# Kernel optimization log

Measured on AMD Instinct MI355X. Metric: run time of the kernel, lower is better.

The kernel has to match this reference:

```python
import jax, jax.numpy as jnp
import numpy as np

EPS = 1e-6      # zero-token detection eps
LN_EPS = 1e-5   # torch LayerNorm default
H = 8           # num_heads


def setup_inputs() -> dict:
    key = jax.random.key(0)
    ks = jax.random.split(key, 6)
    B, T, D = 4, 2048, 512
    embs = jax.random.normal(ks[0], (B, T, D), jnp.float32)
    labels = jax.random.uniform(ks[1], (B, T), jnp.float32)
    s = 1.0 / np.sqrt(D)
    ln_g = jnp.ones((D,), jnp.float32)
    ln_b = jnp.zeros((D,), jnp.float32)
    in_proj_w = jax.random.uniform(ks[2], (3 * D, D), jnp.float32, -s, s)
    in_proj_b = jnp.zeros((3 * D,), jnp.float32)
    out_w = jax.random.uniform(ks[3], (D, D), jnp.float32, -s, s)
    out_b = jnp.zeros((D,), jnp.float32)
    alpha = jnp.float32(1.0)
    beta = jnp.float32(0.0)
    return {"embs": embs, "labels": labels, "ln_g": ln_g, "ln_b": ln_b,
            "in_proj_w": in_proj_w, "in_proj_b": in_proj_b,
            "out_w": out_w, "out_b": out_b, "alpha": alpha, "beta": beta}


def reference(embs, labels, ln_g, ln_b, in_proj_w, in_proj_b, out_w, out_b, alpha, beta):
    B, T, D = embs.shape
    h, dh = H, D // H
    # pre-LayerNorm
    mu = embs.mean(-1, keepdims=True)
    var = ((embs - mu) ** 2).mean(-1, keepdims=True)
    x = (embs - mu) / jnp.sqrt(var + LN_EPS) * ln_g + ln_b
    # key padding mask from all-zero tokens (computed on normalized x, as in source)
    kpm = jnp.abs(x).sum(-1) <= EPS                      # [B,T] bool
    w = jnp.where(kpm, jnp.float32(0.0), labels)         # zero labels on masked tokens
    # fused qkv projection (nn.MultiheadAttention in_proj)
    qkv = x @ in_proj_w.T + in_proj_b                    # [B,T,3D]
    q, k, v = jnp.split(qkv, 3, axis=-1)
    def sp(a):
        return a.reshape(B, T, h, dh).transpose(0, 2, 1, 3)  # [B,h,T,dh]
    q, k, v = sp(q), sp(k), sp(v)
    scores = jnp.einsum('bhqd,bhkd->bhqk', q, k) / np.sqrt(dh)
    # additive label bias: alpha * labels (broadcast over heads & queries) + beta
    scores = scores + (alpha * w[:, None, None, :] + beta)
    # key padding mask -> -inf (use large negative for stability)
    scores = jnp.where(kpm[:, None, None, :], jnp.float32(-1e30), scores)
    a = jax.nn.softmax(scores, axis=-1)
    o = jnp.einsum('bhqk,bhkd->bhqd', a, v).transpose(0, 2, 1, 3).reshape(B, T, D)
    o = o @ out_w.T + out_b
    o = jnp.nan_to_num(o, nan=0.0, posinf=0.0, neginf=0.0)
    # masked mean pool over T
    m = (~kpm)[..., None].astype(o.dtype)                # [B,T,1]
    pooled = (o * m).sum(1) / jnp.maximum(m.sum(1), 1.0)  # [B,D]
    return pooled
```

## Files before the change

### kernel.cpp

```cpp
#include <hip/hip_runtime.h>
#include <math.h>

#define T 2048
#define D 512
#define NH 8
#define DH 64
#define NB 4
#define NTOK (NB * T)
#define LOG2E 1.44269504f
#define QSCALE (0.125f * LOG2E)

using bf16x8 = __attribute__((ext_vector_type(8))) short;
using f32x4  = __attribute__((ext_vector_type(4))) float;

static __device__ __forceinline__ unsigned short f2bf(float f) {
    union { float f; unsigned u; } v; v.f = f;
    unsigned r = v.u + 0x7fffu + ((v.u >> 16) & 1u);
    return (unsigned short)(r >> 16);
}
#if __has_builtin(__builtin_amdgcn_cvt_pk_bf16_f32)
static __device__ __forceinline__ unsigned pack_bf16_pair(float a, float b) {
    auto r = __builtin_amdgcn_cvt_pk_bf16_f32(a, b);
    union { decltype(r) v; unsigned u; } c; c.v = r;
    return c.u;
}
#else
static __device__ __forceinline__ unsigned pack_bf16_pair(float a, float b) {
    union { float f; unsigned u; } ua, ub; ua.f = a; ub.f = b;
    unsigned ra = ua.u + 0x7fffu + ((ua.u >> 16) & 1u);
    unsigned rb = ub.u + 0x7fffu + ((ub.u >> 16) & 1u);
    return __builtin_amdgcn_perm(rb, ra, 0x07060302);
}
#endif


__global__ __launch_bounds__(256) void prep_kernel(
    const float* __restrict__ embs, const float* __restrict__ labels,
    const float* __restrict__ g, const float* __restrict__ bb,
    const float* __restrict__ alpha_p, const float* __restrict__ beta_p,
    const float* __restrict__ ipw,
    unsigned short* __restrict__ xfrag, float* __restrict__ wexp,
    float* __restrict__ kpmf, unsigned short* __restrict__ wbfrag,
    float* __restrict__ S)
{
    __shared__ __align__(16) unsigned short Sh[16][520];
    int blk = blockIdx.x;
    int tid = threadIdx.x, wave = tid >> 6, lane = tid & 63;
    int quad = lane >> 4, lm = lane & 15;

    if (blk >= 608) {
        float4 z = {0.f, 0.f, 0.f, 0.f};
        ((float4*)S)[tid] = z;
        ((float4*)S)[tid + 256] = z;
        return;
    }

    if (blk < 512) {
        int t16 = blk;
        float4 g0 = *(const float4*)(g + lane * 8), g1 = *(const float4*)(g + lane * 8 + 4);
        float4 c0 = *(const float4*)(bb + lane * 8), c1 = *(const float4*)(bb + lane * 8 + 4);
        float gv[8] = {g0.x, g0.y, g0.z, g0.w, g1.x, g1.y, g1.z, g1.w};
        float cv[8] = {c0.x, c0.y, c0.z, c0.w, c1.x, c1.y, c1.z, c1.w};

        for (int tt = 0; tt < 4; ++tt) {
            int n = t16 * 16 + wave * 4 + tt;
            const float* e = embs + (size_t)n * D + lane * 8;
            float4 a4 = *(const float4*)e, b4 = *(const float4*)(e + 4);
            float v[8] = {a4.x, a4.y, a4.z, a4.w, b4.x, b4.y, b4.z, b4.w};

            float s = 0.f, ss = 0.f;
            #pragma unroll
            for (int j = 0; j < 8; ++j) { s += v[j]; ss += v[j] * v[j]; }
            #pragma unroll
            for (int o = 1; o <= 32; o <<= 1) {
                s += __shfl_xor(s, o, 64);
                ss += __shfl_xor(ss, o, 64);
            }
            float mu = s * (1.0f / D);
            float var = ss * (1.0f / D) - mu * mu;
            float rstd = rsqrtf(var + 1e-5f);

            float x[8], as = 0.f;
            #pragma unroll
            for (int j = 0; j < 8; ++j) {
                x[j] = (v[j] - mu) * rstd * gv[j] + cv[j];
                as += fabsf(x[j]);
            }
            uint4 pk;
            pk.x = pack_bf16_pair(x[0], x[1]);
            pk.y = pack_bf16_pair(x[2], x[3]);
            pk.z = pack_bf16_pair(x[4], x[5]);
            pk.w = pack_bf16_pair(x[6], x[7]);
            *(uint4*)&Sh[wave * 4 + tt][lane * 8] = pk;

            #pragma unroll
            for (int o = 1; o <= 32; o <<= 1) as += __shfl_xor(as, o, 64);
            if (lane == 0) {
                int kpm = (as <= 1e-6f);
                kpmf[n] = kpm ? 1.0f : 0.0f;
                wexp[n] = kpm ? 0.0f : __expf(alpha_p[0] * labels[n] + beta_p[0]);
            }
        }
        __syncthreads();
        #pragma unroll
        for (int i = 0; i < 4; ++i) {
            int kc = wave * 4 + i;
            bf16x8 fr = *(const bf16x8*)&Sh[lm][kc * 32 + quad * 8];
            *(bf16x8*)(xfrag + ((size_t)(t16 * 16 + kc) * 64 + lane) * 8) = fr;
        }
    } else {
        int j16 = blk - 512;
        for (int tt = 0; tt < 4; ++tt) {
            int j = j16 * 16 + wave * 4 + tt;
            const float* wp = ipw + (size_t)j * D + lane * 8;
            float4 a4 = *(const float4*)wp, b4 = *(const float4*)(wp + 4);
            uint4 pk;
            pk.x = pack_bf16_pair(a4.x, a4.y);
            pk.y = pack_bf16_pair(a4.z, a4.w);
            pk.z = pack_bf16_pair(b4.x, b4.y);
            pk.w = pack_bf16_pair(b4.z, b4.w);
            *(uint4*)&Sh[wave * 4 + tt][lane * 8] = pk;
        }
        __syncthreads();
        #pragma unroll
        for (int i = 0; i < 4; ++i) {
            int kc = wave * 4 + i;
            bf16x8 fr = *(const bf16x8*)&Sh[lm][kc * 32 + quad * 8];
            *(bf16x8*)(wbfrag + ((size_t)(j16 * 16 + kc) * 64 + lane) * 8) = fr;
        }
    }
}

__global__ __launch_bounds__(256) void qkv_mfma(
    const unsigned short* __restrict__ xfrag, const unsigned short* __restrict__ wbfrag,
    const float* __restrict__ bias, const float* __restrict__ wexp,
    unsigned short* __restrict__ qfrag, unsigned short* __restrict__ kfrag,
    unsigned short* __restrict__ vfrag)
{
    __shared__ __align__(16) unsigned short Ls[4][64][72];
    int tid = threadIdx.x;
    int wave = tid >> 6, lane = tid & 63, quad = lane >> 4, lm = lane & 15;
    int wr = wave >> 1, wc = wave & 1;
    int bid = blockIdx.x;
    int xcd = bid & 7, i = bid >> 3;
    int mblk = xcd * 8 + (i & 7);
    int jblk = i >> 3;
    int m0 = mblk * 128 + wr * 64;
    int j0 = jblk * 128 + wc * 64;
    int mt16 = m0 >> 4, jt16 = j0 >> 4;

    f32x4 acc[4][4];
    #pragma unroll
    for (int a = 0; a < 4; ++a)
        #pragma unroll
        for (int b = 0; b < 4; ++b) acc[a][b] = (f32x4){0.f,0.f,0.f,0.f};

    bf16x8 af0[4], bf0[4], af1[4], bf1[4];
    auto load_ab = [&](int kc, bf16x8 (&af)[4], bf16x8 (&bf)[4]) {
        #pragma unroll
        for (int mf = 0; mf < 4; ++mf)
            af[mf] = *(const bf16x8*)(xfrag + ((size_t)((mt16 + mf) * 16 + kc) * 64 + lane) * 8);
        #pragma unroll
        for (int nt = 0; nt < 4; ++nt)
            bf[nt] = *(const bf16x8*)(wbfrag + ((size_t)((jt16 + nt) * 16 + kc) * 64 + lane) * 8);
    };
    auto do_mfma = [&](bf16x8 (&af)[4], bf16x8 (&bf)[4]) {
        #pragma unroll
        for (int mf = 0; mf < 4; ++mf)
            #pragma unroll
            for (int nt = 0; nt < 4; ++nt)
                acc[mf][nt] = __builtin_amdgcn_mfma_f32_16x16x32_bf16(af[mf], bf[nt], acc[mf][nt], 0, 0, 0);
    };

    load_ab(0, af0, bf0);
    for (int kc = 0; kc < 16; kc += 2) {
        load_ab(kc + 1, af1, bf1);
        do_mfma(af0, bf0);
        load_ab((kc + 2) & 15, af0, bf0);
        do_mfma(af1, bf1);
    }

    int part = j0 >> 9;
    int h = (j0 & 511) >> 6;
    int b_ = m0 >> 11, tloc = m0 & (T - 1);
    int bh = b_ * NH + h;
    float bcol[4];
    #pragma unroll
    for (int nt = 0; nt < 4; ++nt) bcol[nt] = bias[j0 + nt * 16 + lm];

    if (part == 2) {
        float wv[4][4];
        #pragma unroll
        for (int mf = 0; mf < 4; ++mf)
            #pragma unroll
            for (int r = 0; r < 4; ++r)
                wv[mf][r] = wexp[b_ * T + tloc + mf * 16 + quad * 4 + r];
        #pragma unroll
        for (int mf = 0; mf < 4; ++mf)
            #pragma unroll
            for (int nt = 0; nt < 4; ++nt) {
                uint2 pw;
                pw.x = pack_bf16_pair((acc[mf][nt][0] + bcol[nt]) * wv[mf][0],
                                      (acc[mf][nt][1] + bcol[nt]) * wv[mf][1]);
                pw.y = pack_bf16_pair((acc[mf][nt][2] + bcol[nt]) * wv[mf][2],
                                      (acc[mf][nt][3] + bcol[nt]) * wv[mf][3]);
                *(uint2*)&Ls[wave][nt * 16 + lm][mf * 16 + quad * 4] = pw;
            }
        #pragma unroll
        for (int nt = 0; nt < 4; ++nt)
            #pragma unroll
            for (int kk = 0; kk < 2; ++kk) {
                bf16x8 fr = *(const bf16x8*)&Ls[wave][nt * 16 + lm][kk * 32 + quad * 8];
                size_t chunk = ((((size_t)bh * 32 + (tloc >> 6)) * 2 + kk) * 5) + nt;
                *(bf16x8*)(vfrag + chunk * 512 + lane * 8) = fr;
            }
        #pragma unroll
        for (int kk = 0; kk < 2; ++kk) {
            size_t chunk = ((((size_t)bh * 32 + (tloc >> 6)) * 2 + kk) * 5) + 4;
            uint4 pk = {0u, 0u, 0u, 0u};
            if (lm == 0) {
                const float* wp = wexp + b_ * T + tloc + kk * 32 + quad * 8;
                unsigned short vv[8];
                #pragma unroll
                for (int e = 0; e < 8; ++e) vv[e] = f2bf(wp[e]);
                pk = *(uint4*)vv;
            }
            *(uint4*)(vfrag + chunk * 512 + (size_t)lane * 8) = pk;
        }
    } else {
        float scale = (part == 0) ? QSCALE : 1.0f;
        #pragma unroll
        for (int mf = 0; mf < 4; ++mf)
            #pragma unroll
            for (int nt = 0; nt < 4; ++nt)
                #pragma unroll
                for (int r = 0; r < 4; ++r)
                    Ls[wave][mf * 16 + quad * 4 + r][nt * 16 + lm] =
                        f2bf((acc[mf][nt][r] + bcol[nt]) * scale);
        if (part == 0) {
            #pragma unroll
            for (int mf = 0; mf < 4; ++mf)
                #pragma unroll
                for (int kk = 0; kk < 2; ++kk) {
                    bf16x8 fr = *(const bf16x8*)&Ls[wave][mf * 16 + lm][kk * 32 + quad * 8];
                    size_t chunk = ((size_t)bh * 128 + (tloc >> 4) + mf) * 2 + kk;
                    *(bf16x8*)(qfrag + chunk * 512 + lane * 8) = fr;
                }
        } else {
            #pragma unroll
            for (int nta = 0; nta < 4; ++nta)
                #pragma unroll
                for (int kk = 0; kk < 2; ++kk) {
                    bf16x8 fr = *(const bf16x8*)&Ls[wave][lm * 4 + nta][kk * 32 + quad * 8];
                    size_t chunk = ((((size_t)bh * 32 + (tloc >> 6)) * 2 + kk) * 4) + nta;
                    *(bf16x8*)(kfrag + chunk * 512 + lane * 8) = fr;
                }
        }
    }
}

__global__ __launch_bounds__(256, 2) void attn_mfma(
    const unsigned short* __restrict__ qfrag, const unsigned short* __restrict__ kfrag,
    const unsigned short* __restrict__ vfrag, const float* __restrict__ kpmf,
    float* __restrict__ S)
{
    __shared__ __align__(16) unsigned short Ps[4][2][64][72];
    __shared__ float Lx[2][2][64];
    int g = blockIdx.x;
    int bh = g & 31, q0 = (g >> 5) * 128;
    int tid = threadIdx.x, wave = tid >> 6, lane = tid & 63;
    int quad = lane >> 4, lm = lane & 15;
    int qh = wave >> 1, ks = wave & 1;
    int qbase = q0 + qh * 64;
    int b_ = bh >> 3, h = bh & 7;

    bf16x8 qf[4][2];
    int t16b = (qbase >> 4);
    #pragma unroll
    for (int mf = 0; mf < 4; ++mf)
        #pragma unroll
        for (int kk = 0; kk < 2; ++kk)
            qf[mf][kk] = *(const bf16x8*)(qfrag +
                (((size_t)(bh * 128 + t16b + mf) * 2 + kk) * 64 + lane) * 8);

    f32x4 accO[4][4], accL[4];
    #pragma unroll
    for (int mf = 0; mf < 4; ++mf) {
        #pragma unroll
        for (int nt = 0; nt < 4; ++nt) accO[mf][nt] = (f32x4){0.f,0.f,0.f,0.f};
        accL[mf] = (f32x4){0.f,0.f,0.f,0.f};
    }

    const unsigned short* kb = kfrag + (size_t)bh * 32 * 8 * 512 + (size_t)lane * 8;
    const unsigned short* vb = vfrag + (size_t)bh * 32 * 10 * 512 + (size_t)lane * 8;
    int t0k = ks * 16;

    bf16x8 kf[4][2];
    auto load_k = [&](int t64) {
        const unsigned short* p = kb + (size_t)t64 * 8 * 512;
        #pragma unroll
        for (int kk = 0; kk < 2; ++kk)
            #pragma unroll
            for (int nt = 0; nt < 4; ++nt)
                kf[nt][kk] = *(const bf16x8*)(p + ((size_t)kk * 4 + nt) * 512);
    };
    auto load_v = [&](int t64, bf16x8 (&vf)[5][2]) {
        const unsigned short* p = vb + (size_t)t64 * 10 * 512;
        #pragma unroll
        for (int kk = 0; kk < 2; ++kk)
            #pragma unroll
            for (int nt = 0; nt < 5; ++nt)
                vf[nt][kk] = *(const bf16x8*)(p + ((size_t)kk * 5 + nt) * 512);
    };
    auto load_p = [&](int buf, bf16x8 (&pf)[4][2]) {
        #pragma unroll
        for (int mf = 0; mf < 4; ++mf)
            #pragma unroll
            for (int kk = 0; kk < 2; ++kk)
                pf[mf][kk] = *(const bf16x8*)&Ps[wave][buf][mf * 16 + lm][kk * 32 + quad * 8];
    };
    auto qk_exp = [&](int buf) {
        #pragma unroll
        for (int mf = 0; mf < 4; ++mf) {
            f32x4 s[4];
            __builtin_amdgcn_s_setprio(1);
            #pragma unroll
            for (int nt = 0; nt < 4; ++nt) {
                f32x4 t0 = (f32x4){0.f,0.f,0.f,0.f};
                t0 = __builtin_amdgcn_mfma_f32_16x16x32_bf16(qf[mf][0], kf[nt][0], t0, 0, 0, 0);
                t0 = __builtin_amdgcn_mfma_f32_16x16x32_bf16(qf[mf][1], kf[nt][1], t0, 0, 0, 0);
                s[nt] = t0;
            }
            __builtin_amdgcn_s_setprio(0);
            int rowb = mf * 16 + quad * 4;
            #pragma unroll
            for (int r = 0; r < 4; ++r) {
                float p0 = __builtin_amdgcn_exp2f(s[0][r]);
                float p1 = __builtin_amdgcn_exp2f(s[1][r]);
                float p2 = __builtin_amdgcn_exp2f(s[2][r]);
                float p3 = __builtin_amdgcn_exp2f(s[3][r]);
                uint2 pw;
                pw.x = pack_bf16_pair(p0, p1);
                pw.y = pack_bf16_pair(p2, p3);
                *(uint2*)&Ps[wave][buf][rowb + r][lm * 4] = pw;
            }
        }
    };
    auto pv = [&](bf16x8 (&pf)[4][2], bf16x8 (&vf)[5][2]) {
        __builtin_amdgcn_s_setprio(1);
        #pragma unroll
        for (int mf = 0; mf < 4; ++mf) {
            #pragma unroll
            for (int nt = 0; nt < 4; ++nt) {
                accO[mf][nt] = __builtin_amdgcn_mfma_f32_16x16x32_bf16(pf[mf][0], vf[nt][0], accO[mf][nt], 0, 0, 0);
                accO[mf][nt] = __builtin_amdgcn_mfma_f32_16x16x32_bf16(pf[mf][1], vf[nt][1], accO[mf][nt], 0, 0, 0);
            }
            accL[mf] = __builtin_amdgcn_mfma_f32_16x16x32_bf16(pf[mf][0], vf[4][0], accL[mf], 0, 0, 0);
            accL[mf] = __builtin_amdgcn_mfma_f32_16x16x32_bf16(pf[mf][1], vf[4][1], accL[mf], 0, 0, 0);
        }
        __builtin_amdgcn_s_setprio(0);
    };

    load_k(t0k);
    qk_exp(0);
    load_k(t0k + 1);
    for (int t = 1; t < 16; ++t) {
        bf16x8 pf[4][2], vf[5][2];
        load_p((t - 1) & 1, pf);
        load_v(t0k + t - 1, vf);
        qk_exp(t & 1);
        load_k(t0k + ((t + 1) & 15));
        pv(pf, vf);
    }
    {
        bf16x8 pf[4][2], vf[5][2];
        load_p(1, pf);
        load_v(t0k + 15, vf);
        pv(pf, vf);
    }

    if (lm == 0) {
        #pragma unroll
        for (int mf = 0; mf < 4; ++mf)
            #pragma unroll
            for (int r = 0; r < 4; ++r)
                Lx[qh][ks][mf * 16 + quad * 4 + r] = accL[mf][r];
    }
    __syncthreads();

    float pooled[4] = {0.f, 0.f, 0.f, 0.f};
    #pragma unroll
    for (int mf = 0; mf < 4; ++mf)
        #pragma unroll
        for (int r = 0; r < 4; ++r) {
            int rloc = mf * 16 + quad * 4 + r;
            float l = Lx[qh][0][rloc] + Lx[qh][1][rloc];
            float w = (1.0f - kpmf[b_ * T + qbase + rloc]) / l;
            #pragma unroll
            for (int nt = 0; nt < 4; ++nt) pooled[nt] += accO[mf][nt][r] * w;
        }
    #pragma unroll
    for (int nt = 0; nt < 4; ++nt) {
        pooled[nt] += __shfl_xor(pooled[nt], 16, 64);
        pooled[nt] += __shfl_xor(pooled[nt], 32, 64);
    }
    if (quad == 0) {
        #pragma unroll
        for (int nt = 0; nt < 4; ++nt)
            atomicAdd(&S[b_ * D + h * DH + nt * 16 + lm], pooled[nt]);
    }
}

__global__ __launch_bounds__(256) void out_kernel(
    const float* __restrict__ S, const float* __restrict__ kpmf,
    const float* __restrict__ Wo, const float* __restrict__ bo,
    float* __restrict__ out)
{
    __shared__ float Sl[512];
    __shared__ float cs[4];
    __shared__ float pr[4][64];
    int b_ = blockIdx.x >> 3;
    int cg = blockIdx.x & 7;
    int tid = threadIdx.x;
    int col = tid & 63, kq = tid >> 6;
    Sl[tid] = S[b_ * D + tid];
    Sl[tid + 256] = S[b_ * D + tid + 256];
    const float* kp = kpmf + b_ * T;
    float c = 0.f;
    for (int t = tid; t < T; t += 256) c += kp[t];
    #pragma unroll
    for (int o = 32; o; o >>= 1) c += __shfl_xor(c, o, 64);
    if ((tid & 63) == 0) cs[tid >> 6] = c;
    __syncthreads();
    float masked = cs[0] + cs[1] + cs[2] + cs[3];
    float cnt = (float)T - masked;
    float inv = 1.0f / fmaxf(cnt, 1.0f);

    int d = cg * 64 + col;
    const float4* wr4 = (const float4*)(Wo + (size_t)d * D + kq * 128);
    float dot = 0.f;
    #pragma unroll 8
    for (int i = 0; i < 32; ++i) {
        float4 w4 = wr4[i];
        int kbase = kq * 128 + i * 4;
        dot += Sl[kbase + 0] * w4.x + Sl[kbase + 1] * w4.y +
               Sl[kbase + 2] * w4.z + Sl[kbase + 3] * w4.w;
    }
    pr[kq][col] = dot;
    __syncthreads();
    if (kq == 0) {
        float tot = pr[0][col] + pr[1][col] + pr[2][col] + pr[3][col];
        out[b_ * D + d] = (tot + bo[d] * cnt) * inv;
    }
}

extern "C" void kernel_launch(void* const* d_in, const int* in_sizes, int n_in,
                              void* d_out, int out_size, void* d_ws, size_t ws_size,
                              hipStream_t stream) {
    const float* embs   = (const float*)d_in[0];
    const float* labels = (const float*)d_in[1];
    const float* ln_g   = (const float*)d_in[2];
    const float* ln_b   = (const float*)d_in[3];
    const float* ipw    = (const float*)d_in[4];
    const float* ipb    = (const float*)d_in[5];
    const float* ow     = (const float*)d_in[6];
    const float* obb    = (const float*)d_in[7];
    const float* alpha  = (const float*)d_in[8];
    const float* beta   = (const float*)d_in[9];
    float* out = (float*)d_out;

    unsigned short* xfrag  = (unsigned short*)d_ws;
    unsigned short* wbfrag = xfrag + (size_t)NTOK * D;
    unsigned short* qfrag  = wbfrag + (size_t)3 * D * D;
    unsigned short* kfrag  = qfrag + (size_t)NTOK * D;
    unsigned short* vfrag  = kfrag + (size_t)NTOK * D;
    float* wexp = (float*)(vfrag + (size_t)32 * 32 * 2 * 5 * 512);
    float* kpmf = wexp + NTOK;
    float* S    = kpmf + NTOK;

    prep_kernel<<<609, 256, 0, stream>>>(embs, labels, ln_g, ln_b, alpha, beta,
                                         ipw, xfrag, wexp, kpmf, wbfrag, S);
    qkv_mfma<<<768, 256, 0, stream>>>(xfrag, wbfrag, ipb, wexp, qfrag, kfrag, vfrag);
    attn_mfma<<<32 * (T / 128), 256, 0, stream>>>(qfrag, kfrag, vfrag, kpmf, S);
    out_kernel<<<NB * 8, 256, 0, stream>>>(S, kpmf, ow, obb, out);
}
```

Baseline: 153.2 us.

## Fuse four kernels into one persistent mega-kernel with global barriers

Merges the prep, QKV GEMM, attention and output-projection kernels into a single 512-block launch. Stages are separated by atomic-counter grid barriers, and one LDS union is shared across the stages. The QKV stage assigns 1.5 tiles per block, so blocks below 256 do a second unit. The aim is to remove kernel launch gaps and inter-kernel drain/fill. The risks are deadlock if not all 512 blocks are co-resident, imbalance in the QKV stage, and barrier spin overhead; it also adds a memset.

```diff
diff --git a/kernel.cpp b/kernel.cpp
--- a/kernel.cpp
+++ b/kernel.cpp
@@ -34,28 +34,47 @@
 #endif
 
 
-__global__ __launch_bounds__(256) void prep_kernel(
+struct AttnLds { unsigned short Ps[4][2][64][72]; float Lx[2][2][64]; };
+struct OutLds  { float Sl[512]; float cs[4]; float pr[4][64]; };
+union MegaLds {
+    unsigned short Sh[16][520];
+    unsigned short Ls[4][64][72];
+    AttnLds at;
+    OutLds  op;
+};
+
+__global__ __launch_bounds__(256, 2) void mega_kernel(
     const float* __restrict__ embs, const float* __restrict__ labels,
     const float* __restrict__ g, const float* __restrict__ bb,
     const float* __restrict__ alpha_p, const float* __restrict__ beta_p,
-    const float* __restrict__ ipw,
-    unsigned short* __restrict__ xfrag, float* __restrict__ wexp,
-    float* __restrict__ kpmf, unsigned short* __restrict__ wbfrag,
-    float* __restrict__ S)
+    const float* __restrict__ ipw, const float* __restrict__ ipb,
+    const float* __restrict__ ow, const float* __restrict__ obb,
+    unsigned short* __restrict__ xfrag, unsigned short* __restrict__ wbfrag,
+    unsigned short* __restrict__ qfrag, unsigned short* __restrict__ kfrag,
+    unsigned short* __restrict__ vfrag,
+    float* __restrict__ wexp, float* __restrict__ kpmf,
+    float* S, int* cnt, float* __restrict__ out)
 {
-    __shared__ __align__(16) unsigned short Sh[16][520];
+    __shared__ __align__(16) MegaLds u;
     int blk = blockIdx.x;
     int tid = threadIdx.x, wave = tid >> 6, lane = tid & 63;
     int quad = lane >> 4, lm = lane & 15;
 
-    if (blk >= 608) {
-        float4 z = {0.f, 0.f, 0.f, 0.f};
-        ((float4*)S)[tid] = z;
-        ((float4*)S)[tid + 256] = z;
-        return;
-    }
-
-    if (blk < 512) {
+    auto gsync = [&](int idx, bool wait) {
+        __syncthreads();
+        __threadfence();
+        if (tid == 0) {
+            __hip_atomic_fetch_add(&cnt[idx], 1, __ATOMIC_ACQ_REL, __HIP_MEMORY_SCOPE_AGENT);
+            if (wait) {
+                while (__hip_atomic_load(&cnt[idx], __ATOMIC_ACQUIRE, __HIP_MEMORY_SCOPE_AGENT) < 512)
+                    __builtin_amdgcn_s_sleep(8);
+            }
+        }
+        __syncthreads();
+        __threadfence();
+    };
+
+    {
         int t16 = blk;
         float4 g0 = *(const float4*)(g + lane * 8), g1 = *(const float4*)(g + lane * 8 + 4);
         float4 c0 = *(const float4*)(bb + lane * 8), c1 = *(const float4*)(bb + lane * 8 + 4);
@@ -91,7 +110,7 @@
             pk.y = pack_bf16_pair(x[2], x[3]);
             pk.z = pack_bf16_pair(x[4], x[5]);
             pk.w = pack_bf16_pair(x[6], x[7]);
-            *(uint4*)&Sh[wave * 4 + tt][lane * 8] = pk;
+            *(uint4*)&u.Sh[wave * 4 + tt][lane * 8] = pk;
 
             #pragma unroll
             for (int o = 1; o <= 32; o <<= 1) as += __shfl_xor(as, o, 64);
@@ -105,352 +124,337 @@
         #pragma unroll
         for (int i = 0; i < 4; ++i) {
             int kc = wave * 4 + i;
-            bf16x8 fr = *(const bf16x8*)&Sh[lm][kc * 32 + quad * 8];
+            bf16x8 fr = *(const bf16x8*)&u.Sh[lm][kc * 32 + quad * 8];
             *(bf16x8*)(xfrag + ((size_t)(t16 * 16 + kc) * 64 + lane) * 8) = fr;
         }
-    } else {
-        int j16 = blk - 512;
-        for (int tt = 0; tt < 4; ++tt) {
-            int j = j16 * 16 + wave * 4 + tt;
-            const float* wp = ipw + (size_t)j * D + lane * 8;
-            float4 a4 = *(const float4*)wp, b4 = *(const float4*)(wp + 4);
-            uint4 pk;
-            pk.x = pack_bf16_pair(a4.x, a4.y);
-            pk.y = pack_bf16_pair(a4.z, a4.w);
-            pk.z = pack_bf16_pair(b4.x, b4.y);
-            pk.w = pack_bf16_pair(b4.z, b4.w);
-            *(uint4*)&Sh[wave * 4 + tt][lane * 8] = pk;
-        }
-        __syncthreads();
-        #pragma unroll
-        for (int i = 0; i < 4; ++i) {
-            int kc = wave * 4 + i;
-            bf16x8 fr = *(const bf16x8*)&Sh[lm][kc * 32 + quad * 8];
-            *(bf16x8*)(wbfrag + ((size_t)(j16 * 16 + kc) * 64 + lane) * 8) = fr;
+
+        if (blk < 96) {
+            __syncthreads();
+            int j16 = blk;
+            for (int tt = 0; tt < 4; ++tt) {
+                int j = j16 * 16 + wave * 4 + tt;
+                const float* wp = ipw + (size_t)j * D + lane * 8;
+                float4 a4 = *(const float4*)wp, b4 = *(const float4*)(wp + 4);
+                uint4 pk;
+                pk.x = pack_bf16_pair(a4.x, a4.y);
+                pk.y = pack_bf16_pair(a4.z, a4.w);
+                pk.z = pack_bf16_pair(b4.x, b4.y);
+                pk.w = pack_bf16_pair(b4.z, b4.w);
+                *(uint4*)&u.Sh[wave * 4 + tt][lane * 8] = pk;
+            }
+            __syncthreads();
+            #pragma unroll
+            for (int i = 0; i < 4; ++i) {
+                int kc = wave * 4 + i;
+                bf16x8 fr = *(const bf16x8*)&u.Sh[lm][kc * 32 + quad * 8];
+                *(bf16x8*)(wbfrag + ((size_t)(j16 * 16 + kc) * 64 + lane) * 8) = fr;
+            }
         }
     }
-}
-
-__global__ __launch_bounds__(256) void qkv_mfma(
-    const unsigned short* __restrict__ xfrag, const unsigned short* __restrict__ wbfrag,
-    const float* __restrict__ bias, const float* __restrict__ wexp,
-    unsigned short* __restrict__ qfrag, unsigned short* __restrict__ kfrag,
-    unsigned short* __restrict__ vfrag)
-{
-    __shared__ __align__(16) unsigned short Ls[4][64][72];
-    int tid = threadIdx.x;
-    int wave = tid >> 6, lane = tid & 63, quad = lane >> 4, lm = lane & 15;
-    int wr = wave >> 1, wc = wave & 1;
-    int bid = blockIdx.x;
-    int xcd = bid & 7, i = bid >> 3;
-    int mblk = xcd * 8 + (i & 7);
-    int jblk = i >> 3;
-    int m0 = mblk * 128 + wr * 64;
-    int j0 = jblk * 128 + wc * 64;
-    int mt16 = m0 >> 4, jt16 = j0 >> 4;
-
-    f32x4 acc[4][4];
-    #pragma unroll
-    for (int a = 0; a < 4; ++a)
-        #pragma unroll
-        for (int b = 0; b < 4; ++b) acc[a][b] = (f32x4){0.f,0.f,0.f,0.f};
-
-    bf16x8 af0[4], bf0[4], af1[4], bf1[4];
-    auto load_ab = [&](int kc, bf16x8 (&af)[4], bf16x8 (&bf)[4]) {
+    gsync(0, true);
+
+    {
+        int wr = wave >> 1, wc = wave & 1;
+        auto qkv_unit = [&](int unit) {
+            int xcd = unit & 7, i = unit >> 3;
+            int mblk = xcd * 8 + (i & 7);
+            int jblk = i >> 3;
+            int m0 = mblk * 128 + wr * 64;
+            int j0 = jblk * 128 + wc * 64;
+            int mt16 = m0 >> 4, jt16 = j0 >> 4;
+
+            f32x4 acc[4][4];
+            #pragma unroll
+            for (int a = 0; a < 4; ++a)
+                #pragma unroll
+                for (int b = 0; b < 4; ++b) acc[a][b] = (f32x4){0.f,0.f,0.f,0.f};
+
+            bf16x8 af0[4], bf0[4], af1[4], bf1[4];
+            auto load_ab = [&](int kc, bf16x8 (&af)[4], bf16x8 (&bf)[4]) {
+                #pragma unroll
+                for (int mf = 0; mf < 4; ++mf)
+                    af[mf] = *(const bf16x8*)(xfrag + ((size_t)((mt16 + mf) * 16 + kc) * 64 + lane) * 8);
+                #pragma unroll
+                for (int nt = 0; nt < 4; ++nt)
+                    bf[nt] = *(const bf16x8*)(wbfrag + ((size_t)((jt16 + nt) * 16 + kc) * 64 + lane) * 8);
+            };
+            auto do_mfma = [&](bf16x8 (&af)[4], bf16x8 (&bf)[4]) {
+                #pragma unroll
+                for (int mf = 0; mf < 4; ++mf)
+                    #pragma unroll
+                    for (int nt = 0; nt < 4; ++nt)
+                        acc[mf][nt] = __builtin_amdgcn_mfma_f32_16x16x32_bf16(af[mf], bf[nt], acc[mf][nt], 0, 0, 0);
+            };
+
+            load_ab(0, af0, bf0);
+            for (int kc = 0; kc < 16; kc += 2) {
+                load_ab(kc + 1, af1, bf1);
+                do_mfma(af0, bf0);
+                load_ab((kc + 2) & 15, af0, bf0);
+                do_mfma(af1, bf1);
+            }
+
+            int part = j0 >> 9;
+            int h = (j0 & 511) >> 6;
+            int b_ = m0 >> 11, tloc = m0 & (T - 1);
+            int bh = b_ * NH + h;
+            float bcol[4];
+            #pragma unroll
+            for (int nt = 0; nt < 4; ++nt) bcol[nt] = ipb[j0 + nt * 16 + lm];
+
+            if (part == 2) {
+                float wv[4][4];
+                #pragma unroll
+                for (int mf = 0; mf < 4; ++mf)
+                    #pragma unroll
+                    for (int r = 0; r < 4; ++r)
+                        wv[mf][r] = wexp[b_ * T + tloc + mf * 16 + quad * 4 + r];
+                #pragma unroll
+                for (int mf = 0; mf < 4; ++mf)
+                    #pragma unroll
+                    for (int nt = 0; nt < 4; ++nt) {
+                        uint2 pw;
+                        pw.x = pack_bf16_pair((acc[mf][nt][0] + bcol[nt]) * wv[mf][0],
+                                              (acc[mf][nt][1] + bcol[nt]) * wv[mf][1]);
+                        pw.y = pack_bf16_pair((acc[mf][nt][2] + bcol[nt]) * wv[mf][2],
+                                              (acc[mf][nt][3] + bcol[nt]) * wv[mf][3]);
+                        *(uint2*)&u.Ls[wave][nt * 16 + lm][mf * 16 + quad * 4] = pw;
+                    }
+                #pragma unroll
+                for (int nt = 0; nt < 4; ++nt)
+                    #pragma unroll
+                    for (int kk = 0; kk < 2; ++kk) {
+                        bf16x8 fr = *(const bf16x8*)&u.Ls[wave][nt * 16 + lm][kk * 32 + quad * 8];
+                        size_t chunk = ((((size_t)bh * 32 + (tloc >> 6)) * 2 + kk) * 5) + nt;
+                        *(bf16x8*)(vfrag + chunk * 512 + lane * 8) = fr;
+                    }
+                #pragma unroll
+                for (int kk = 0; kk < 2; ++kk) {
+                    size_t chunk = ((((size_t)bh * 32 + (tloc >> 6)) * 2 + kk) * 5) + 4;
+                    uint4 pk = {0u, 0u, 0u, 0u};
+                    if (lm == 0) {
+                        const float* wp = wexp + b_ * T + tloc + kk * 32 + quad * 8;
+                        unsigned short vv[8];
+                        #pragma unroll
+                        for (int e = 0; e < 8; ++e) vv[e] = f2bf(wp[e]);
+                        pk = *(uint4*)vv;
+                    }
+                    *(uint4*)(vfrag + chunk * 512 + (size_t)lane * 8) = pk;
+                }
+            } else {
+                float scale = (part == 0) ? QSCALE : 1.0f;
+                #pragma unroll
+                for (int mf = 0; mf < 4; ++mf)
+                    #pragma unroll
+                    for (int nt = 0; nt < 4; ++nt)
+                        #pragma unroll
+                        for (int r = 0; r < 4; ++r)
+                            u.Ls[wave][mf * 16 + quad * 4 + r][nt * 16 + lm] =
+                                f2bf((acc[mf][nt][r] + bcol[nt]) * scale);
+                if (part == 0) {
+                    #pragma unroll
+                    for (int mf = 0; mf < 4; ++mf)
+                        #pragma unroll
+                        for (int kk = 0; kk < 2; ++kk) {
+                            bf16x8 fr = *(const bf16x8*)&u.Ls[wave][mf * 16 + lm][kk * 32 + quad * 8];
+                            size_t chunk = ((size_t)bh * 128 + (tloc >> 4) + mf) * 2 + kk;
+                            *(bf16x8*)(qfrag + chunk * 512 + lane * 8) = fr;
+                        }
+                } else {
+                    #pragma unroll
+                    for (int nta = 0; nta < 4; ++nta)
+                        #pragma unroll
+                        for (int kk = 0; kk < 2; ++kk) {
+                            bf16x8 fr = *(const bf16x8*)&u.Ls[wave][lm * 4 + nta][kk * 32 + quad * 8];
+                            size_t chunk = ((((size_t)bh * 32 + (tloc >> 6)) * 2 + kk) * 4) + nta;
+                            *(bf16x8*)(kfrag + chunk * 512 + lane * 8) = fr;
+                        }
+                }
+            }
+        };
+        qkv_unit(blk);
+        if (blk < 256) { __syncthreads(); qkv_unit(blk + 512); }
+    }
+    gsync(1, true);
+
+    {
+        int bh = blk & 31, q0 = (blk >> 5) * 128;
+        int qh = wave >> 1, ks = wave & 1;
+        int qbase = q0 + qh * 64;
+        int b_ = bh >> 3, h = bh & 7;
+
+        bf16x8 qf[4][2];
+        int t16b = (qbase >> 4);
         #pragma unroll
         for (int mf = 0; mf < 4; ++mf)
-            af[mf] = *(const bf16x8*)(xfrag + ((size_t)((mt16 + mf) * 16 + kc) * 64 + lane) * 8);
-        #pragma unroll
-        for (int nt = 0; nt < 4; ++nt)
-            bf[nt] = *(const bf16x8*)(wbfrag + ((size_t)((jt16 + nt) * 16 + kc) * 64 + lane) * 8);
-    };
-    auto do_mfma = [&](bf16x8 (&af)[4], bf16x8 (&bf)[4]) {
+            #pragma unroll
+            for (int kk = 0; kk < 2; ++kk)
+                qf[mf][kk] = *(const bf16x8*)(qfrag +
+                    (((size_t)(bh * 128 + t16b + mf) * 2 + kk) * 64 + lane) * 8);
+
+        f32x4 accO[4][4], accL[4];
+        #pragma unroll
+        for (int mf = 0; mf < 4; ++mf) {
+            #pragma unroll
+            for (int nt = 0; nt < 4; ++nt) accO[mf][nt] = (f32x4){0.f,0.f,0.f,0.f};
+            accL[mf] = (f32x4){0.f,0.f,0.f,0.f};
+        }
+
+        const unsigned short* kb = kfrag + (size_t)bh * 32 * 8 * 512 + (size_t)lane * 8;
+        const unsigned short* vb = vfrag + (size_t)bh * 32 * 10 * 512 + (size_t)lane * 8;
+        int t0k = ks * 16;
+
+        bf16x8 kf[4][2];
+        auto load_k = [&](int t64) {
+            const unsigned short* p = kb + (size_t)t64 * 8 * 512;
+            #pragma unroll
+            for (int kk = 0; kk < 2; ++kk)
+                #pragma unroll
+                for (int nt = 0; nt < 4; ++nt)
+                    kf[nt][kk] = *(const bf16x8*)(p + ((size_t)kk * 4 + nt) * 512);
+        };
+        auto load_v = [&](int t64, bf16x8 (&vf)[5][2]) {
+            const unsigned short* p = vb + (size_t)t64 * 10 * 512;
+            #pragma unroll
+            for (int kk = 0; kk < 2; ++kk)
+                #pragma unroll
+                for (int nt = 0; nt < 5; ++nt)
+                    vf[nt][kk] = *(const bf16x8*)(p + ((size_t)kk * 5 + nt) * 512);
+        };
+        auto load_p = [&](int buf, bf16x8 (&pf)[4][2]) {
+            #pragma unroll
+            for (int mf = 0; mf < 4; ++mf)
+                #pragma unroll
+                for (int kk = 0; kk < 2; ++kk)
+                    pf[mf][kk] = *(const bf16x8*)&u.at.Ps[wave][buf][mf * 16 + lm][kk * 32 + quad * 8];
+        };
+        auto qk_exp = [&](int buf) {
+            #pragma unroll
+            for (int mf = 0; mf < 4; ++mf) {
+                f32x4 s[4];
+                __builtin_amdgcn_s_setprio(1);
+                #pragma unroll
+                for (int nt = 0; nt < 4; ++nt) {
+                    f32x4 t0 = (f32x4){0.f,0.f,0.f,0.f};
+                    t0 = __builtin_amdgcn_mfma_f32_16x16x32_bf16(qf[mf][0], kf[nt][0], t0, 0, 0, 0);
+                    t0 = __builtin_amdgcn_mfma_f32_16x16x32_bf16(qf[mf][1], kf[nt][1], t0, 0, 0, 0);
+                    s[nt] = t0;
+                }
+                __builtin_amdgcn_s_setprio(0);
+                int rowb = mf * 16 + quad * 4;
+                #pragma unroll
+                for (int r = 0; r < 4; ++r) {
+                    float p0 = __builtin_amdgcn_exp2f(s[0][r]);
+                    float p1 = __builtin_amdgcn_exp2f(s[1][r]);
+                    float p2 = __builtin_amdgcn_exp2f(s[2][r]);
+                    float p3 = __builtin_amdgcn_exp2f(s[3][r]);
+                    uint2 pw;
+                    pw.x = pack_bf16_pair(p0, p1);
+                    pw.y = pack_bf16_pair(p2, p3);
+                    *(uint2*)&u.at.Ps[wave][buf][rowb + r][lm * 4] = pw;
+                }
+            }
+        };
+        auto pv = [&](bf16x8 (&pf)[4][2], bf16x8 (&vf)[5][2]) {
+            __builtin_amdgcn_s_setprio(1);
+            #pragma unroll
+            for (int mf = 0; mf < 4; ++mf) {
+                #pragma unroll
+                for (int nt = 0; nt < 4; ++nt) {
+                    accO[mf][nt] = __builtin_amdgcn_mfma_f32_16x16x32_bf16(pf[mf][0], vf[nt][0], accO[mf][nt], 0, 0, 0);
+                    accO[mf][nt] = __builtin_amdgcn_mfma_f32_16x16x32_bf16(pf[mf][1], vf[nt][1], accO[mf][nt], 0, 0, 0);
+                }
+                accL[mf] = __builtin_amdgcn_mfma_f32_16x16x32_bf16(pf[mf][0], vf[4][0], accL[mf], 0, 0, 0);
+                accL[mf] = __builtin_amdgcn_mfma_f32_16x16x32_bf16(pf[mf][1], vf[4][1], accL[mf], 0, 0, 0);
+            }
+            __builtin_amdgcn_s_setprio(0);
+        };
+
+        load_k(t0k);
+        qk_exp(0);
+        load_k(t0k + 1);
+        for (int t = 1; t < 16; ++t) {
+            bf16x8 pf[4][2], vf[5][2];
+            load_p((t - 1) & 1, pf);
+            load_v(t0k + t - 1, vf);
+            qk_exp(t & 1);
+            load_k(t0k + ((t + 1) & 15));
+            pv(pf, vf);
+        }
+        {
+            bf16x8 pf[4][2], vf[5][2];
+            load_p(1, pf);
+            load_v(t0k + 15, vf);
+            pv(pf, vf);
+        }
+
+        if (lm == 0) {
+            #pragma unroll
+            for (int mf = 0; mf < 4; ++mf)
+                #pragma unroll
+                for (int r = 0; r < 4; ++r)
+                    u.at.Lx[qh][ks][mf * 16 + quad * 4 + r] = accL[mf][r];
+        }
+        __syncthreads();
+
+        float pooled[4] = {0.f, 0.f, 0.f, 0.f};
         #pragma unroll
         for (int mf = 0; mf < 4; ++mf)
             #pragma unroll
+            for (int r = 0; r < 4; ++r) {
+                int rloc = mf * 16 + quad * 4 + r;
+                float l = u.at.Lx[qh][0][rloc] + u.at.Lx[qh][1][rloc];
+                float w = (1.0f - kpmf[b_ * T + qbase + rloc]) / l;
+                #pragma unroll
+                for (int nt = 0; nt < 4; ++nt) pooled[nt] += accO[mf][nt][r] * w;
+            }
+        #pragma unroll
+        for (int nt = 0; nt < 4; ++nt) {
+            pooled[nt] += __shfl_xor(pooled[nt], 16, 64);
+            pooled[nt] += __shfl_xor(pooled[nt], 32, 64);
+        }
+        if (quad == 0) {
+            #pragma unroll
             for (int nt = 0; nt < 4; ++nt)
-                acc[mf][nt] = __builtin_amdgcn_mfma_f32_16x16x32_bf16(af[mf], bf[nt], acc[mf][nt], 0, 0, 0);
-    };
-
-    load_ab(0, af0, bf0);
-    for (int kc = 0; kc < 16; kc += 2) {
-        load_ab(kc + 1, af1, bf1);
-        do_mfma(af0, bf0);
-        load_ab((kc + 2) & 15, af0, bf0);
-        do_mfma(af1, bf1);
+                atomicAdd(&S[b_ * D + h * DH + nt * 16 + lm], pooled[nt]);
+        }
     }
 
-    int part = j0 >> 9;
-    int h = (j0 & 511) >> 6;
-    int b_ = m0 >> 11, tloc = m0 & (T - 1);
-    int bh = b_ * NH + h;
-    float bcol[4];
-    #pragma unroll
-    for (int nt = 0; nt < 4; ++nt) bcol[nt] = bias[j0 + nt * 16 + lm];
-
-    if (part == 2) {
-        float wv[4][4];
-        #pragma unroll
-        for (int mf = 0; mf < 4; ++mf)
-            #pragma unroll
-            for (int r = 0; r < 4; ++r)
-                wv[mf][r] = wexp[b_ * T + tloc + mf * 16 + quad * 4 + r];
-        #pragma unroll
-        for (int mf = 0; mf < 4; ++mf)
-            #pragma unroll
-            for (int nt = 0; nt < 4; ++nt) {
-                uint2 pw;
-                pw.x = pack_bf16_pair((acc[mf][nt][0] + bcol[nt]) * wv[mf][0],
-                                      (acc[mf][nt][1] + bcol[nt]) * wv[mf][1]);
-                pw.y = pack_bf16_pair((acc[mf][nt][2] + bcol[nt]) * wv[mf][2],
-                                      (acc[mf][nt][3] + bcol[nt]) * wv[mf][3]);
-                *(uint2*)&Ls[wave][nt * 16 + lm][mf * 16 + quad * 4] = pw;
-            }
-        #pragma unroll
-        for (int nt = 0; nt < 4; ++nt)
-            #pragma unroll
-            for (int kk = 0; kk < 2; ++kk) {
-                bf16x8 fr = *(const bf16x8*)&Ls[wave][nt * 16 + lm][kk * 32 + quad * 8];
-                size_t chunk = ((((size_t)bh * 32 + (tloc >> 6)) * 2 + kk) * 5) + nt;
-                *(bf16x8*)(vfrag + chunk * 512 + lane * 8) = fr;
-            }
-        #pragma unroll
-        for (int kk = 0; kk < 2; ++kk) {
-            size_t chunk = ((((size_t)bh * 32 + (tloc >> 6)) * 2 + kk) * 5) + 4;
-            uint4 pk = {0u, 0u, 0u, 0u};
-            if (lm == 0) {
-                const float* wp = wexp + b_ * T + tloc + kk * 32 + quad * 8;
-                unsigned short vv[8];
-                #pragma unroll
-                for (int e = 0; e < 8; ++e) vv[e] = f2bf(wp[e]);
-                pk = *(uint4*)vv;
-            }
-            *(uint4*)(vfrag + chunk * 512 + (size_t)lane * 8) = pk;
-        }
-    } else {
-        float scale = (part == 0) ? QSCALE : 1.0f;
-        #pragma unroll
-        for (int mf = 0; mf < 4; ++mf)
-            #pragma unroll
-            for (int nt = 0; nt < 4; ++nt)
-                #pragma unroll
-                for (int r = 0; r < 4; ++r)
-                    Ls[wave][mf * 16 + quad * 4 + r][nt * 16 + lm] =
-                        f2bf((acc[mf][nt][r] + bcol[nt]) * scale);
-        if (part == 0) {
-            #pragma unroll
-            for (int mf = 0; mf < 4; ++mf)
-                #pragma unroll
-                for (int kk = 0; kk < 2; ++kk) {
-                    bf16x8 fr = *(const bf16x8*)&Ls[wave][mf * 16 + lm][kk * 32 + quad * 8];
-                    size_t chunk = ((size_t)bh * 128 + (tloc >> 4) + mf) * 2 + kk;
-                    *(bf16x8*)(qfrag + chunk * 512 + lane * 8) = fr;
-                }
-        } else {
-            #pragma unroll
-            for (int nta = 0; nta < 4; ++nta)
-                #pragma unroll
-                for (int kk = 0; kk < 2; ++kk) {
-                    bf16x8 fr = *(const bf16x8*)&Ls[wave][lm * 4 + nta][kk * 32 + quad * 8];
-                    size_t chunk = ((((size_t)bh * 32 + (tloc >> 6)) * 2 + kk) * 4) + nta;
-                    *(bf16x8*)(kfrag + chunk * 512 + lane * 8) = fr;
-                }
-        }
-    }
-}
-
-__global__ __launch_bounds__(256, 2) void attn_mfma(
-    const unsigned short* __restrict__ qfrag, const unsigned short* __restrict__ kfrag,
-    const unsigned short* __restrict__ vfrag, const float* __restrict__ kpmf,
-    float* __restrict__ S)
-{
-    __shared__ __align__(16) unsigned short Ps[4][2][64][72];
-    __shared__ float Lx[2][2][64];
-    int g = blockIdx.x;
-    int bh = g & 31, q0 = (g >> 5) * 128;
-    int tid = threadIdx.x, wave = tid >> 6, lane = tid & 63;
-    int quad = lane >> 4, lm = lane & 15;
-    int qh = wave >> 1, ks = wave & 1;
-    int qbase = q0 + qh * 64;
-    int b_ = bh >> 3, h = bh & 7;
-
-    bf16x8 qf[4][2];
-    int t16b = (qbase >> 4);
-    #pragma unroll
-    for (int mf = 0; mf < 4; ++mf)
-        #pragma unroll
-        for (int kk = 0; kk < 2; ++kk)
-            qf[mf][kk] = *(const bf16x8*)(qfrag +
-                (((size_t)(bh * 128 + t16b + mf) * 2 + kk) * 64 + lane) * 8);
-
-    f32x4 accO[4][4], accL[4];
-    #pragma unroll
-    for (int mf = 0; mf < 4; ++mf) {
-        #pragma unroll
-        for (int nt = 0; nt < 4; ++nt) accO[mf][nt] = (f32x4){0.f,0.f,0.f,0.f};
-        accL[mf] = (f32x4){0.f,0.f,0.f,0.f};
-    }
-
-    const unsigned short* kb = kfrag + (size_t)bh * 32 * 8 * 512 + (size_t)lane * 8;
-    const unsigned short* vb = vfrag + (size_t)bh * 32 * 10 * 512 + (size_t)lane * 8;
-    int t0k = ks * 16;
-
-    bf16x8 kf[4][2];
-    auto load_k = [&](int t64) {
-        const unsigned short* p = kb + (size_t)t64 * 8 * 512;
-        #pragma unroll
-        for (int kk = 0; kk < 2; ++kk)
-            #pragma unroll
-            for (int nt = 0; nt < 4; ++nt)
-                kf[nt][kk] = *(const bf16x8*)(p + ((size_t)kk * 4 + nt) * 512);
-    };
-    auto load_v = [&](int t64, bf16x8 (&vf)[5][2]) {
-        const unsigned short* p = vb + (size_t)t64 * 10 * 512;
-        #pragma unroll
-        for (int kk = 0; kk < 2; ++kk)
-            #pragma unroll
-            for (int nt = 0; nt < 5; ++nt)
-                vf[nt][kk] = *(const bf16x8*)(p + ((size_t)kk * 5 + nt) * 512);
-    };
-    auto load_p = [&](int buf, bf16x8 (&pf)[4][2]) {
-        #pragma unroll
-        for (int mf = 0; mf < 4; ++mf)
-            #pragma unroll
-            for (int kk = 0; kk < 2; ++kk)
-                pf[mf][kk] = *(const bf16x8*)&Ps[wave][buf][mf * 16 + lm][kk * 32 + quad * 8];
-    };
-    auto qk_exp = [&](int buf) {
-        #pragma unroll
-        for (int mf = 0; mf < 4; ++mf) {
-            f32x4 s[4];
-            __builtin_amdgcn_s_setprio(1);
-            #pragma unroll
-            for (int nt = 0; nt < 4; ++nt) {
-                f32x4 t0 = (f32x4){0.f,0.f,0.f,0.f};
-                t0 = __builtin_amdgcn_mfma_f32_16x16x32_bf16(qf[mf][0], kf[nt][0], t0, 0, 0, 0);
-                t0 = __builtin_amdgcn_mfma_f32_16x16x32_bf16(qf[mf][1], kf[nt][1], t0, 0, 0, 0);
-                s[nt] = t0;
-            }
-            __builtin_amdgcn_s_setprio(0);
-            int rowb = mf * 16 + quad * 4;
-            #pragma unroll
-            for (int r = 0; r < 4; ++r) {
-                float p0 = __builtin_amdgcn_exp2f(s[0][r]);
-                float p1 = __builtin_amdgcn_exp2f(s[1][r]);
-                float p2 = __builtin_amdgcn_exp2f(s[2][r]);
-                float p3 = __builtin_amdgcn_exp2f(s[3][r]);
-                uint2 pw;
-                pw.x = pack_bf16_pair(p0, p1);
-                pw.y = pack_bf16_pair(p2, p3);
-                *(uint2*)&Ps[wave][buf][rowb + r][lm * 4] = pw;
-            }
-        }
-    };
-    auto pv = [&](bf16x8 (&pf)[4][2], bf16x8 (&vf)[5][2]) {
-        __builtin_amdgcn_s_setprio(1);
-        #pragma unroll
-        for (int mf = 0; mf < 4; ++mf) {
-            #pragma unroll
-            for (int nt = 0; nt < 4; ++nt) {
-                accO[mf][nt] = __builtin_amdgcn_mfma_f32_16x16x32_bf16(pf[mf][0], vf[nt][0], accO[mf][nt], 0, 0, 0);
-                accO[mf][nt] = __builtin_amdgcn_mfma_f32_16x16x32_bf16(pf[mf][1], vf[nt][1], accO[mf][nt], 0, 0, 0);
-            }
-            accL[mf] = __builtin_amdgcn_mfma_f32_16x16x32_bf16(pf[mf][0], vf[4][0], accL[mf], 0, 0, 0);
-            accL[mf] = __builtin_amdgcn_mfma_f32_16x16x32_bf16(pf[mf][1], vf[4][1], accL[mf], 0, 0, 0);
-        }
-        __builtin_amdgcn_s_setprio(0);
-    };
-
-    load_k(t0k);
-    qk_exp(0);
-    load_k(t0k + 1);
-    for (int t = 1; t < 16; ++t) {
-        bf16x8 pf[4][2], vf[5][2];
-        load_p((t - 1) & 1, pf);
-        load_v(t0k + t - 1, vf);
-        qk_exp(t & 1);
-        load_k(t0k + ((t + 1) & 15));
-        pv(pf, vf);
-    }
+    if (blk >= 32) { gsync(2, false); return; }
+    gsync(2, true);
     {
-        bf16x8 pf[4][2], vf[5][2];
-        load_p(1, pf);
-        load_v(t0k + 15, vf);
-        pv(pf, vf);
-    }
-
-    if (lm == 0) {
-        #pragma unroll
-        for (int mf = 0; mf < 4; ++mf)
-            #pragma unroll
-            for (int r = 0; r < 4; ++r)
-                Lx[qh][ks][mf * 16 + quad * 4 + r] = accL[mf][r];
-    }
-    __syncthreads();
-
-    float pooled[4] = {0.f, 0.f, 0.f, 0.f};
-    #pragma unroll
-    for (int mf = 0; mf < 4; ++mf)
-        #pragma unroll
-        for (int r = 0; r < 4; ++r) {
-            int rloc = mf * 16 + quad * 4 + r;
-            float l = Lx[qh][0][rloc] + Lx[qh][1][rloc];
-            float w = (1.0f - kpmf[b_ * T + qbase + rloc]) / l;
-            #pragma unroll
-            for (int nt = 0; nt < 4; ++nt) pooled[nt] += accO[mf][nt][r] * w;
-        }
-    #pragma unroll
-    for (int nt = 0; nt < 4; ++nt) {
-        pooled[nt] += __shfl_xor(pooled[nt], 16, 64);
-        pooled[nt] += __shfl_xor(pooled[nt], 32, 64);
-    }
-    if (quad == 0) {
-        #pragma unroll
-        for (int nt = 0; nt < 4; ++nt)
-            atomicAdd(&S[b_ * D + h * DH + nt * 16 + lm], pooled[nt]);
-    }
-}
-
-__global__ __launch_bounds__(256) void out_kernel(
-    const float* __restrict__ S, const float* __restrict__ kpmf,
-    const float* __restrict__ Wo, const float* __restrict__ bo,
-    float* __restrict__ out)
-{
-    __shared__ float Sl[512];
-    __shared__ float cs[4];
-    __shared__ float pr[4][64];
-    int b_ = blockIdx.x >> 3;
-    int cg = blockIdx.x & 7;
-    int tid = threadIdx.x;
-    int col = tid & 63, kq = tid >> 6;
-    Sl[tid] = S[b_ * D + tid];
-    Sl[tid + 256] = S[b_ * D + tid + 256];
-    const float* kp = kpmf + b_ * T;
-    float c = 0.f;
-    for (int t = tid; t < T; t += 256) c += kp[t];
-    #pragma unroll
-    for (int o = 32; o; o >>= 1) c += __shfl_xor(c, o, 64);
-    if ((tid & 63) == 0) cs[tid >> 6] = c;
-    __syncthreads();
-    float masked = cs[0] + cs[1] + cs[2] + cs[3];
-    float cnt = (float)T - masked;
-    float inv = 1.0f / fmaxf(cnt, 1.0f);
-
-    int d = cg * 64 + col;
-    const float4* wr4 = (const float4*)(Wo + (size_t)d * D + kq * 128);
-    float dot = 0.f;
-    #pragma unroll 8
-    for (int i = 0; i < 32; ++i) {
-        float4 w4 = wr4[i];
-        int kbase = kq * 128 + i * 4;
-        dot += Sl[kbase + 0] * w4.x + Sl[kbase + 1] * w4.y +
-               Sl[kbase + 2] * w4.z + Sl[kbase + 3] * w4.w;
-    }
-    pr[kq][col] = dot;
-    __syncthreads();
-    if (kq == 0) {
-        float tot = pr[0][col] + pr[1][col] + pr[2][col] + pr[3][col];
-        out[b_ * D + d] = (tot + bo[d] * cnt) * inv;
+        int b_ = blk >> 3;
+        int cg = blk & 7;
+        int col = tid & 63, kq = tid >> 6;
+        u.op.Sl[tid] = S[b_ * D + tid];
+        u.op.Sl[tid + 256] = S[b_ * D + tid + 256];
+        const float* kp = kpmf + b_ * T;
+        float c = 0.f;
+        for (int t = tid; t < T; t += 256) c += kp[t];
+        #pragma unroll
+        for (int o = 32; o; o >>= 1) c += __shfl_xor(c, o, 64);
+        if ((tid & 63) == 0) u.op.cs[tid >> 6] = c;
+        __syncthreads();
+        float masked = u.op.cs[0] + u.op.cs[1] + u.op.cs[2] + u.op.cs[3];
+        float cnt_ = (float)T - masked;
+        float inv = 1.0f / fmaxf(cnt_, 1.0f);
+
+        int d = cg * 64 + col;
+        const float4* wr4 = (const float4*)(ow + (size_t)d * D + kq * 128);
+        float dot = 0.f;
+        #pragma unroll 8
+        for (int i = 0; i < 32; ++i) {
+            float4 w4 = wr4[i];
+            int kbase = kq * 128 + i * 4;
+            dot += u.op.Sl[kbase + 0] * w4.x + u.op.Sl[kbase + 1] * w4.y +
+                   u.op.Sl[kbase + 2] * w4.z + u.op.Sl[kbase + 3] * w4.w;
+        }
+        u.op.pr[kq][col] = dot;
+        __syncthreads();
+        if (kq == 0) {
+            float tot = u.op.pr[0][col] + u.op.pr[1][col] + u.op.pr[2][col] + u.op.pr[3][col];
+            out[b_ * D + d] = (tot + obb[d] * cnt_) * inv;
+        }
     }
 }
 
@@ -477,10 +481,11 @@
     float* wexp = (float*)(vfrag + (size_t)32 * 32 * 2 * 5 * 512);
     float* kpmf = wexp + NTOK;
     float* S    = kpmf + NTOK;
-
-    prep_kernel<<<609, 256, 0, stream>>>(embs, labels, ln_g, ln_b, alpha, beta,
-                                         ipw, xfrag, wexp, kpmf, wbfrag, S);
-    qkv_mfma<<<768, 256, 0, stream>>>(xfrag, wbfrag, ipb, wexp, qfrag, kfrag, vfrag);
-    attn_mfma<<<32 * (T / 128), 256, 0, stream>>>(qfrag, kfrag, vfrag, kpmf, S);
-    out_kernel<<<NB * 8, 256, 0, stream>>>(S, kpmf, ow, obb, out);
+    int*   cnt  = (int*)(S + NB * D);
+
+    hipMemsetAsync(S, 0, (size_t)NB * D * sizeof(float) + 4 * sizeof(int), stream);
+    mega_kernel<<<512, 256, 0, stream>>>(embs, labels, ln_g, ln_b, alpha, beta,
+                                         ipw, ipb, ow, obb,
+                                         xfrag, wbfrag, qfrag, kfrag, vfrag,
+                                         wexp, kpmf, S, cnt, out);
 }
```

Measured after the change: 526.2 us. 244% more time.
